# Optimization experiments

Measured on AMD Instinct MI355X. Metric: run time of the kernel, lower is better.

Reference implementation:

```python
import jax, jax.numpy as jnp
import numpy as np

F_DIM, H, O = 128, 256, 256
NQ, EQ = 64, 512
ND, ED = 50000, 600000

PARAM_SHAPES = [
    ("qW1", (F_DIM, H)), ("qb1", (H,)), ("qW2", (H, H)), ("qb2", (H,)),
    ("qW3", (H, H)),     ("qb3", (H,)), ("qW4", (H, O)), ("qb4", (O,)),
    ("dW1", (F_DIM, H)), ("db1", (H,)), ("dW2", (H, H)), ("db2", (H,)),
    ("dW3", (H, H)),     ("db3", (H,)), ("dW4", (H, O)), ("db4", (O,)),
    ("lW1", (2 * O, O)), ("lb1", (O,)),
    ("lW2", (O, O // 2)), ("lb2", (O // 2,)),
    ("lW3", (O // 2, 8)), ("lb3", (8,)),
]

def setup_inputs() -> dict:
    key = jax.random.key(0)
    ks = jax.random.split(key, 4 + len(PARAM_SHAPES))
    inp = {
        "query_in_feat": jax.random.normal(ks[0], (NQ, F_DIM), jnp.float32),
        "data_in_feat": jax.random.normal(ks[1], (ND, F_DIM), jnp.float32),
        "query_edge_list": jax.random.randint(ks[2], (2, EQ), 0, NQ),
        "data_edge_list": jax.random.randint(ks[3], (2, ED), 0, ND),
    }
    for i, (name, shape) in enumerate(PARAM_SHAPES):
        fan_in = shape[0] if len(shape) == 2 else 1
        inp[name] = jax.random.normal(ks[4 + i], shape, jnp.float32) * (1.0 / np.sqrt(fan_in))
    return inp

def _mlp2(x, W1, b1, W2, b2):
    return jnp.maximum(x @ W1 + b1, 0.0) @ W2 + b2

def _gin_conv(x, src, dst, W1, b1, W2, b2):
    # GINConv (eps=0): MLP(x_i + sum_{j->i} x_j); gather x[src], scatter-add at dst
    agg = jax.ops.segment_sum(x[src], dst, num_segments=x.shape[0])
    return _mlp2(x + agg, W1, b1, W2, b2)

def _gin(x, edge_index, p):
    src, dst = edge_index[0], edge_index[1]
    h = jnp.maximum(_gin_conv(x, src, dst, *p[:4]), 0.0)  # ReLU between convs
    return _gin_conv(h, src, dst, *p[4:])

def reference(query_in_feat, data_in_feat, query_edge_list, data_edge_list,
              qW1, qb1, qW2, qb2, qW3, qb3, qW4, qb4,
              dW1, db1, dW2, db2, dW3, db3, dW4, db4,
              lW1, lb1, lW2, lb2, lW3, lb3):
    qx = _gin(query_in_feat, query_edge_list, (qW1, qb1, qW2, qb2, qW3, qb3, qW4, qb4))
    dx = _gin(data_in_feat, data_edge_list, (dW1, db1, dW2, db2, dW3, db3, dW4, db4))
    # global_add_pool with batch = zeros -> single-graph sum
    qp = jnp.sum(qx, axis=0, keepdims=True)  # [1, O]
    dp = jnp.sum(dx, axis=0, keepdims=True)  # [1, O]
    h = jnp.concatenate([qp, dp], axis=1)    # [1, 2*O]
    h = jnp.maximum(h @ lW1 + lb1, 0.0)
    h = jnp.maximum(h @ lW2 + lb2, 0.0)
    h = jnp.maximum(h @ lW3 + lb3, 0.0)
    return h.reshape(1, 8)
```

## Files before the change

kernel.cpp:

```cpp
#include <hip/hip_runtime.h>
#include <hip/hip_bf16.h>


#define NQ 64
#define EQ 512
#define ND 50000
#define ED 600000
#define FDIM 128
#define HDIM 256

typedef __attribute__((ext_vector_type(8))) short short8;
typedef __attribute__((ext_vector_type(4))) float f32x4;
typedef __attribute__((ext_vector_type(4))) unsigned short us4;
typedef __attribute__((ext_vector_type(2))) unsigned short us2;

__device__ __forceinline__ unsigned short f2bf(float f) {
    union { float f; unsigned u; } v; v.f = f;
    unsigned r = v.u + 0x7FFF + ((v.u >> 16) & 1);
    return (unsigned short)(r >> 16);
}
__device__ __forceinline__ float bf2f(unsigned short u) {
    union { unsigned u; float f; } v; v.u = ((unsigned)u) << 16;
    return v.f;
}


__global__ void cvt_to_bf16(const float* __restrict__ xd, const float* __restrict__ xq,
                            unsigned short* __restrict__ out, long long nd4, long long n4) {
    long long i = (long long)blockIdx.x * 256 + threadIdx.x;
    if (i >= n4) return;
    const float* src = (i < nd4) ? (xd + i * 4) : (xq + (i - nd4) * 4);
    float4 v = *(const float4*)src;
    us4 o;
    o[0] = f2bf(v.x); o[1] = f2bf(v.y); o[2] = f2bf(v.z); o[3] = f2bf(v.w);
    *(us4*)(out + i * 4) = o;
}


__global__ void count_deg_both(const int* __restrict__ d_dst, int* __restrict__ d_deg,
                               const int* __restrict__ q_dst, int* __restrict__ q_deg,
                               int dblocks) {
    int b = blockIdx.x;
    if (b < dblocks) {
        int e = b * 256 + threadIdx.x;
        if (e < ED) atomicAdd(&d_deg[d_dst[e]], 1);
    } else {
        int e = (b - dblocks) * 256 + threadIdx.x;
        if (e < EQ) atomicAdd(&q_deg[q_dst[e]], 1);
    }
}

__device__ __forceinline__ void scan1_body(const int* deg, int* rowptr, int* bsum,
                                           int n, int blk) {
    __shared__ int sh[256];
    const int t = threadIdx.x;
    const int i = blk * 256 + t;
    const int v = (i < n) ? deg[i] : 0;
    sh[t] = v;
    __syncthreads();
    for (int off = 1; off < 256; off <<= 1) {
        int x = (t >= off) ? sh[t - off] : 0;
        __syncthreads();
        sh[t] += x;
        __syncthreads();
    }
    if (i < n) rowptr[i] = sh[t] - v;
    if (t == 255) bsum[blk] = sh[255];
}

__global__ void scan_phase1_both(const int* __restrict__ d_deg, int* __restrict__ d_rowptr,
                                 int* __restrict__ d_bsum,
                                 const int* __restrict__ q_deg, int* __restrict__ q_rowptr,
                                 int* __restrict__ q_bsum, int dblocks) {
    int b = blockIdx.x;
    if (b < dblocks) scan1_body(d_deg, d_rowptr, d_bsum, ND, b);
    else             scan1_body(q_deg, q_rowptr, q_bsum, NQ, b - dblocks);
}

__device__ __forceinline__ void scan2_body(const int* bsum, int* boff, int* rowptr_n, int nb) {
    __shared__ int sh[256];
    const int t = threadIdx.x;
    const int v = (t < nb) ? bsum[t] : 0;
    sh[t] = v;
    __syncthreads();
    for (int off = 1; off < 256; off <<= 1) {
        int x = (t >= off) ? sh[t - off] : 0;
        __syncthreads();
        sh[t] += x;
        __syncthreads();
    }
    if (t < nb) boff[t] = sh[t] - v;
    if (t == 255) *rowptr_n = sh[255];
}

__global__ void scan_phase2_both(const int* __restrict__ d_bsum, int* __restrict__ d_boff,
                                 int* __restrict__ d_rowptr_n, int d_nb,
                                 const int* __restrict__ q_bsum, int* __restrict__ q_boff,
                                 int* __restrict__ q_rowptr_n, int q_nb) {
    if (blockIdx.x == 0) scan2_body(d_bsum, d_boff, d_rowptr_n, d_nb);
    else                 scan2_body(q_bsum, q_boff, q_rowptr_n, q_nb);
}

__global__ void scan_phase3_both(int* __restrict__ d_rowptr, const int* __restrict__ d_boff,
                                 int* __restrict__ d_cursor,
                                 int* __restrict__ q_rowptr, const int* __restrict__ q_boff,
                                 int* __restrict__ q_cursor, int dblocks) {
    int b = blockIdx.x;
    if (b < dblocks) {
        int i = b * 256 + threadIdx.x;
        if (i < ND) {
            int r = d_rowptr[i] + d_boff[b];
            d_rowptr[i] = r; d_cursor[i] = r;
        }
    } else {
        int i = (b - dblocks) * 256 + threadIdx.x;
        if (i < NQ) {
            int r = q_rowptr[i] + q_boff[b - dblocks];
            q_rowptr[i] = r; q_cursor[i] = r;
        }
    }
}

__global__ void fill_csr_both(const int* __restrict__ d_src, const int* __restrict__ d_dst,
                              int* __restrict__ d_cursor, int* __restrict__ d_csrsrc,
                              const int* __restrict__ q_src, const int* __restrict__ q_dst,
                              int* __restrict__ q_cursor, int* __restrict__ q_csrsrc,
                              int dblocks) {
    int b = blockIdx.x;
    if (b < dblocks) {
        int e = b * 256 + threadIdx.x;
        if (e < ED) {
            int p = atomicAdd(&d_cursor[d_dst[e]], 1);
            d_csrsrc[p] = d_src[e];
        }
    } else {
        int e = (b - dblocks) * 256 + threadIdx.x;
        if (e < EQ) {
            int p = atomicAdd(&q_cursor[q_dst[e]], 1);
            q_csrsrc[p] = q_src[e];
        }
    }
}


template <int F>
__global__ void gin_agg_dual(const unsigned short* __restrict__ xd, const int* __restrict__ rpd,
                             const int* __restrict__ csd, unsigned short* __restrict__ od,
                             const unsigned short* __restrict__ xq, const int* __restrict__ rpq,
                             const int* __restrict__ csq, unsigned short* __restrict__ oq) {
    constexpr int V = F / 64;
    const unsigned short* x; const int* rowptr; const int* csr; unsigned short* out; int node;
    if ((int)blockIdx.x < ND) { x = xd; rowptr = rpd; csr = csd; out = od; node = blockIdx.x; }
    else { x = xq; rowptr = rpq; csr = csq; out = oq; node = blockIdx.x - ND; }

    const int t = threadIdx.x;
    const int beg = rowptr[node];
    const int end = rowptr[node + 1];

    float acc[V];
    {
        const unsigned short* p = x + (size_t)node * F + t * V;
        if constexpr (V == 4) {
            us4 v = *(const us4*)p;
#pragma unroll
            for (int i = 0; i < 4; ++i) acc[i] = bf2f(v[i]);
        } else {
            us2 v = *(const us2*)p;
            acc[0] = bf2f(v[0]); acc[1] = bf2f(v[1]);
        }
    }
    int j = beg;
    for (; j + 1 < end; j += 2) {
        const unsigned short* p0 = x + (size_t)csr[j] * F + t * V;
        const unsigned short* p1 = x + (size_t)csr[j + 1] * F + t * V;
        if constexpr (V == 4) {
            us4 v0 = *(const us4*)p0;
            us4 v1 = *(const us4*)p1;
#pragma unroll
            for (int i = 0; i < 4; ++i) acc[i] += bf2f(v0[i]) + bf2f(v1[i]);
        } else {
            us2 v0 = *(const us2*)p0;
            us2 v1 = *(const us2*)p1;
            acc[0] += bf2f(v0[0]) + bf2f(v1[0]);
            acc[1] += bf2f(v0[1]) + bf2f(v1[1]);
        }
    }
    if (j < end) {
        const unsigned short* p0 = x + (size_t)csr[j] * F + t * V;
        if constexpr (V == 4) {
            us4 v0 = *(const us4*)p0;
#pragma unroll
            for (int i = 0; i < 4; ++i) acc[i] += bf2f(v0[i]);
        } else {
            us2 v0 = *(const us2*)p0;
            acc[0] += bf2f(v0[0]); acc[1] += bf2f(v0[1]);
        }
    }
    unsigned short* po = out + (size_t)node * F + t * V;
    if constexpr (V == 4) {
        us4 r;
#pragma unroll
        for (int i = 0; i < 4; ++i) r[i] = f2bf(acc[i]);
        *(us4*)po = r;
    } else {
        us2 r; r[0] = f2bf(acc[0]); r[1] = f2bf(acc[1]);
        *(us2*)po = r;
    }
}


struct PackDesc {
    const float* W[8];
    unsigned short* Wp[8];
    int KT[8];
    int start[9];
};

__global__ void pack_all(PackDesc pd) {
    int b = blockIdx.x;
    int m = 0;
    while (m < 7 && b >= pd.start[m + 1]) ++m;
    const int local = b - pd.start[m];
    const int KT = pd.KT[m];
    const int kt = local % KT;
    const int ct = local / KT;
    const float* W = pd.W[m];
    unsigned short* Wp = pd.Wp[m];
    const int l = threadIdx.x;
    const int row = kt * 32 + (l >> 4) * 8;
    const int col = ct * 16 + (l & 15);
    short8 v;
#pragma unroll
    for (int j = 0; j < 8; ++j) v[j] = (short)f2bf(W[(size_t)(row + j) * 256 + col]);
    *(short8*)(Wp + (((size_t)(ct * KT + kt)) * 64 + l) * 8) = v;
}


template <int KIN>
__global__ __launch_bounds__(256) void mlp_dual(
    const unsigned short* __restrict__ Ad,
    const unsigned short* __restrict__ W1pd, const float* __restrict__ b1d,
    const unsigned short* __restrict__ W2pd, const float* __restrict__ b2d,
    unsigned short* __restrict__ Cd, float* __restrict__ poold, int ndb,
    const unsigned short* __restrict__ Aq,
    const unsigned short* __restrict__ W1pq, const float* __restrict__ b1q,
    const unsigned short* __restrict__ W2pq, const float* __restrict__ b2q,
    unsigned short* __restrict__ Cq, float* __restrict__ poolq,
    int relu_out) {
    constexpr int KT1 = KIN / 32;
    __shared__ __align__(16) unsigned short lds[64 * 256];

    const unsigned short* A; const unsigned short* W1p; const float* b1;
    const unsigned short* W2p; const float* b2;
    unsigned short* C; float* pool; int row0, N;
    if ((int)blockIdx.x < ndb) {
        A = Ad; W1p = W1pd; b1 = b1d; W2p = W2pd; b2 = b2d;
        C = Cd; pool = poold; row0 = blockIdx.x * 64; N = ND;
    } else {
        A = Aq; W1p = W1pq; b1 = b1q; W2p = W2pq; b2 = b2q;
        C = Cq; pool = poolq; row0 = 0; N = NQ;
    }

    const int tid = threadIdx.x;
    const int lane = tid & 63;
    const int wv = tid >> 6;
    const int lrow = lane & 15;
    const int lk2 = (lane >> 4) * 8;
    const int nrows = (N - row0 < 64) ? (N - row0) : 64;

    for (int idx = tid; idx < nrows * (KIN / 8); idx += 256) {
        const int r = idx / (KIN / 8);
        const int k8 = (idx % (KIN / 8)) * 8;
        short8 v = *(const short8*)(A + (size_t)(row0 + r) * KIN + k8);
        unsigned byte = (unsigned)((r * KIN + k8) * 2) ^ (unsigned)((r & 7) << 4);
        *(short8*)((char*)lds + byte) = v;
    }
    __syncthreads();

    f32x4 acc1[4][4];
#pragma unroll
    for (int fm = 0; fm < 4; ++fm)
#pragma unroll
        for (int fn = 0; fn < 4; ++fn) acc1[fm][fn] = (f32x4)(0.f);

    const unsigned short* W1Base = W1p + ((size_t)(wv * 4) * KT1 * 64 + lane) * 8;
    for (int kt = 0; kt < KT1; ++kt) {
        short8 a[4], bf[4];
#pragma unroll
        for (int fm = 0; fm < 4; ++fm) {
            const int r = fm * 16 + lrow;
            unsigned byte = (unsigned)((r * KIN + kt * 32 + lk2) * 2) ^ (unsigned)((r & 7) << 4);
            a[fm] = *(const short8*)((const char*)lds + byte);
        }
#pragma unroll
        for (int fn = 0; fn < 4; ++fn)
            bf[fn] = *(const short8*)(W1Base + ((size_t)fn * KT1 + kt) * 64 * 8);
#pragma unroll
        for (int fm = 0; fm < 4; ++fm)
#pragma unroll
            for (int fn = 0; fn < 4; ++fn)
                acc1[fm][fn] = __builtin_amdgcn_mfma_f32_16x16x32_bf16(
                    a[fm], bf[fn], acc1[fm][fn], 0, 0, 0);
    }
    __syncthreads();

#pragma unroll
    for (int fn = 0; fn < 4; ++fn) {
        const int col = wv * 64 + fn * 16 + lrow;
        const float bv = b1[col];
#pragma unroll
        for (int fm = 0; fm < 4; ++fm) {
            const int rbase = fm * 16 + (lane >> 4) * 4;
#pragma unroll
            for (int r = 0; r < 4; ++r) {
                const int row = rbase + r;
                const float v = fmaxf(acc1[fm][fn][r] + bv, 0.f);
                unsigned byte = (unsigned)((row * 256 + col) * 2) ^ (unsigned)((row & 7) << 4);
                *(unsigned short*)((char*)lds + byte) = f2bf(v);
            }
        }
    }
    __syncthreads();

    f32x4 acc2[4][4];
#pragma unroll
    for (int fm = 0; fm < 4; ++fm)
#pragma unroll
        for (int fn = 0; fn < 4; ++fn) acc2[fm][fn] = (f32x4)(0.f);

    const unsigned short* W2Base = W2p + ((size_t)(wv * 4) * 8 * 64 + lane) * 8;
    for (int kt = 0; kt < 8; ++kt) {
        short8 a[4], bf[4];
#pragma unroll
        for (int fm = 0; fm < 4; ++fm) {
            const int r = fm * 16 + lrow;
            unsigned byte = (unsigned)((r * 256 + kt * 32 + lk2) * 2) ^ (unsigned)((r & 7) << 4);
            a[fm] = *(const short8*)((const char*)lds + byte);
        }
#pragma unroll
        for (int fn = 0; fn < 4; ++fn)
            bf[fn] = *(const short8*)(W2Base + ((size_t)fn * 8 + kt) * 64 * 8);
#pragma unroll
        for (int fm = 0; fm < 4; ++fm)
#pragma unroll
            for (int fn = 0; fn < 4; ++fn)
                acc2[fm][fn] = __builtin_amdgcn_mfma_f32_16x16x32_bf16(
                    a[fm], bf[fn], acc2[fm][fn], 0, 0, 0);
    }

#pragma unroll
    for (int fn = 0; fn < 4; ++fn) {
        const int col = wv * 64 + fn * 16 + lrow;
        const float bv = b2[col];
        float ps = 0.f;
#pragma unroll
        for (int fm = 0; fm < 4; ++fm) {
            const int rbase = row0 + fm * 16 + (lane >> 4) * 4;
#pragma unroll
            for (int r = 0; r < 4; ++r) {
                const int row = rbase + r;
                if (row < N) {
                    float v = acc2[fm][fn][r] + bv;
                    if (relu_out) v = fmaxf(v, 0.f);
                    if (C) C[(size_t)row * 256 + col] = f2bf(v);
                    ps += v;
                }
            }
        }
        if (pool) {
            ps += __shfl_xor(ps, 16);
            ps += __shfl_xor(ps, 32);
            if ((lane >> 4) == 0) atomicAdd(&pool[col], ps);
        }
    }
}


__global__ void mlp_head(const float* __restrict__ pooled,
                         const float* __restrict__ lW1, const float* __restrict__ lb1,
                         const float* __restrict__ lW2, const float* __restrict__ lb2,
                         const float* __restrict__ lW3, const float* __restrict__ lb3,
                         float* __restrict__ out) {
    __shared__ float h0[512];
    __shared__ float h1[256];
    __shared__ float h2[128];
    const int t = threadIdx.x;
    h0[t] = pooled[t];
    h0[t + 256] = pooled[t + 256];
    __syncthreads();

    float acc = lb1[t];
    for (int k = 0; k < 512; ++k) acc += h0[k] * lW1[k * 256 + t];
    h1[t] = fmaxf(acc, 0.f);
    __syncthreads();

    if (t < 128) {
        float a = lb2[t];
        for (int k = 0; k < 256; ++k) a += h1[k] * lW2[k * 128 + t];
        h2[t] = fmaxf(a, 0.f);
    }
    __syncthreads();

    if (t < 8) {
        float a = lb3[t];
        for (int k = 0; k < 128; ++k) a += h2[k] * lW3[k * 8 + t];
        out[t] = fmaxf(a, 0.f);
    }
}


extern "C" void kernel_launch(void* const* d_in, const int* in_sizes, int n_in,
                              void* d_out, int out_size, void* d_ws, size_t ws_size,
                              hipStream_t stream) {
    const float* q_x  = (const float*)d_in[0];
    const float* d_x  = (const float*)d_in[1];
    const int*   q_el = (const int*)d_in[2];
    const int*   d_el = (const int*)d_in[3];
    const float* qW1 = (const float*)d_in[4];  const float* qb1 = (const float*)d_in[5];
    const float* qW2 = (const float*)d_in[6];  const float* qb2 = (const float*)d_in[7];
    const float* qW3 = (const float*)d_in[8];  const float* qb3 = (const float*)d_in[9];
    const float* qW4 = (const float*)d_in[10]; const float* qb4 = (const float*)d_in[11];
    const float* dW1 = (const float*)d_in[12]; const float* db1 = (const float*)d_in[13];
    const float* dW2 = (const float*)d_in[14]; const float* db2 = (const float*)d_in[15];
    const float* dW3 = (const float*)d_in[16]; const float* db3 = (const float*)d_in[17];
    const float* dW4 = (const float*)d_in[18]; const float* db4 = (const float*)d_in[19];
    const float* lW1 = (const float*)d_in[20]; const float* lb1 = (const float*)d_in[21];
    const float* lW2 = (const float*)d_in[22]; const float* lb2 = (const float*)d_in[23];
    const float* lW3 = (const float*)d_in[24]; const float* lb3 = (const float*)d_in[25];
    (void)in_sizes; (void)n_in; (void)out_size; (void)ws_size;

    const int* q_src = q_el;  const int* q_dst = q_el + EQ;
    const int* d_src = d_el;  const int* d_dst = d_el + ED;

    char* wsb = (char*)d_ws;
    size_t off = 0;
    auto alloc = [&](size_t bytes) { void* p = wsb + off; off += (bytes + 255) & ~(size_t)255; return p; };

    unsigned short* bxd = (unsigned short*)alloc((size_t)ND * FDIM * 2);
    unsigned short* bxq = (unsigned short*)alloc((size_t)NQ * FDIM * 2);
    unsigned short* dag = (unsigned short*)alloc((size_t)ND * FDIM * 2);
    unsigned short* qag = (unsigned short*)alloc((size_t)NQ * FDIM * 2);
    unsigned short* hd  = (unsigned short*)alloc((size_t)ND * HDIM * 2);
    unsigned short* hq  = (unsigned short*)alloc((size_t)NQ * HDIM * 2);
    unsigned short* had = (unsigned short*)alloc((size_t)ND * HDIM * 2);
    unsigned short* haq = (unsigned short*)alloc((size_t)NQ * HDIM * 2);
    float* pooled = (float*)alloc(512 * 4);
    int* d_deg    = (int*)alloc((size_t)ND * 4);
    int* q_deg    = (int*)alloc((size_t)NQ * 4);
    int* d_rowptr = (int*)alloc((size_t)(ND + 1) * 4);
    int* d_cursor = (int*)alloc((size_t)ND * 4);
    int* d_csrsrc = (int*)alloc((size_t)ED * 4);
    int* d_bsum   = (int*)alloc(256 * 4);
    int* d_boff   = (int*)alloc(256 * 4);
    int* q_rowptr = (int*)alloc((size_t)(NQ + 1) * 4);
    int* q_cursor = (int*)alloc((size_t)NQ * 4);
    int* q_csrsrc = (int*)alloc((size_t)EQ * 4);
    int* q_bsum   = (int*)alloc(256 * 4);
    int* q_boff   = (int*)alloc(256 * 4);
    unsigned short* pdW1 = (unsigned short*)alloc((size_t)FDIM * 256 * 2);
    unsigned short* pdW2 = (unsigned short*)alloc((size_t)HDIM * 256 * 2);
    unsigned short* pdW3 = (unsigned short*)alloc((size_t)HDIM * 256 * 2);
    unsigned short* pdW4 = (unsigned short*)alloc((size_t)HDIM * 256 * 2);
    unsigned short* pqW1 = (unsigned short*)alloc((size_t)FDIM * 256 * 2);
    unsigned short* pqW2 = (unsigned short*)alloc((size_t)HDIM * 256 * 2);
    unsigned short* pqW3 = (unsigned short*)alloc((size_t)HDIM * 256 * 2);
    unsigned short* pqW4 = (unsigned short*)alloc((size_t)HDIM * 256 * 2);

    hipMemsetAsync(pooled, 0, 512 * 4, stream);
    hipMemsetAsync(d_deg, 0, (char*)(q_deg + NQ) - (char*)d_deg, stream);

    {
        long long nd4 = (long long)ND * FDIM / 4;
        long long n4 = nd4 + (long long)NQ * FDIM / 4;
        cvt_to_bf16<<<(int)((n4 + 255) / 256), 256, 0, stream>>>(d_x, q_x, bxd, nd4, n4);
    }

    {
        PackDesc pd;
        const float* Ws[8] = {dW1, dW2, dW3, dW4, qW1, qW2, qW3, qW4};
        unsigned short* Wps[8] = {pdW1, pdW2, pdW3, pdW4, pqW1, pqW2, pqW3, pqW4};
        int kts[8] = {4, 8, 8, 8, 4, 8, 8, 8};
        int s = 0;
        for (int i = 0; i < 8; ++i) {
            pd.W[i] = Ws[i]; pd.Wp[i] = Wps[i]; pd.KT[i] = kts[i];
            pd.start[i] = s; s += 16 * kts[i];
        }
        pd.start[8] = s;
        pack_all<<<s, 64, 0, stream>>>(pd);
    }

    const int d_eb = (ED + 255) / 256;
    const int q_eb = (EQ + 255) / 256;
    const int d_nb = (ND + 255) / 256;
    const int q_nb = (NQ + 255) / 256;
    count_deg_both<<<d_eb + q_eb, 256, 0, stream>>>(d_dst, d_deg, q_dst, q_deg, d_eb);
    scan_phase1_both<<<d_nb + q_nb, 256, 0, stream>>>(d_deg, d_rowptr, d_bsum,
                                                      q_deg, q_rowptr, q_bsum, d_nb);
    scan_phase2_both<<<2, 256, 0, stream>>>(d_bsum, d_boff, d_rowptr + ND, d_nb,
                                            q_bsum, q_boff, q_rowptr + NQ, q_nb);
    scan_phase3_both<<<d_nb + q_nb, 256, 0, stream>>>(d_rowptr, d_boff, d_cursor,
                                                      q_rowptr, q_boff, q_cursor, d_nb);
    fill_csr_both<<<d_eb + q_eb, 256, 0, stream>>>(d_src, d_dst, d_cursor, d_csrsrc,
                                                   q_src, q_dst, q_cursor, q_csrsrc, d_eb);

    const int ndb = (ND + 63) / 64;

    gin_agg_dual<FDIM><<<ND + NQ, 64, 0, stream>>>(bxd, d_rowptr, d_csrsrc, dag,
                                                   bxq, q_rowptr, q_csrsrc, qag);
    mlp_dual<FDIM><<<ndb + 1, 256, 0, stream>>>(
        dag, pdW1, db1, pdW2, db2, hd, nullptr, ndb,
        qag, pqW1, qb1, pqW2, qb2, hq, nullptr, 1);

    gin_agg_dual<HDIM><<<ND + NQ, 64, 0, stream>>>(hd, d_rowptr, d_csrsrc, had,
                                                   hq, q_rowptr, q_csrsrc, haq);
    mlp_dual<HDIM><<<ndb + 1, 256, 0, stream>>>(
        had, pdW3, db3, pdW4, db4, nullptr, pooled + 256, ndb,
        haq, pqW3, qb3, pqW4, qb4, nullptr, pooled, 0);

    mlp_head<<<1, 256, 0, stream>>>(pooled, lW1, lb1, lW2, lb2, lW3, lb3, (float*)d_out);
}
```

Before: 260.9 us.

## Store hidden activations as FP8 and fuse prepass kernels into one launch

The intermediate hidden features between the two GIN layers are now stored as FP8 (one byte per element) instead of bf16. A new aggregation kernel gathers and sums them with packed fp8-to-f32 conversion, which halves the bytes moved in the memory-bound neighbor gather and in the MLP output write. Separately, feature conversion, weight packing and degree counting are merged into a single prepass launch to cut launch overhead. FP8 storage of activations loses precision and may push accuracy toward the tolerance limit, and the MLP now writes single bytes per lane, which is less coalesced.

```diff
diff --git a/kernel.cpp b/kernel.cpp
--- a/kernel.cpp
+++ b/kernel.cpp
@@ -11,6 +11,7 @@
 
 typedef __attribute__((ext_vector_type(8))) short short8;
 typedef __attribute__((ext_vector_type(4))) float f32x4;
+typedef __attribute__((ext_vector_type(2))) float floatx2;
 typedef __attribute__((ext_vector_type(4))) unsigned short us4;
 typedef __attribute__((ext_vector_type(2))) unsigned short us2;
 
@@ -25,30 +26,62 @@
 }
 
 
-__global__ void cvt_to_bf16(const float* __restrict__ xd, const float* __restrict__ xq,
-                            unsigned short* __restrict__ out, long long nd4, long long n4) {
-    long long i = (long long)blockIdx.x * 256 + threadIdx.x;
-    if (i >= n4) return;
-    const float* src = (i < nd4) ? (xd + i * 4) : (xq + (i - nd4) * 4);
-    float4 v = *(const float4*)src;
-    us4 o;
-    o[0] = f2bf(v.x); o[1] = f2bf(v.y); o[2] = f2bf(v.z); o[3] = f2bf(v.w);
-    *(us4*)(out + i * 4) = o;
-}
-
-
-__global__ void count_deg_both(const int* __restrict__ d_dst, int* __restrict__ d_deg,
-                               const int* __restrict__ q_dst, int* __restrict__ q_deg,
-                               int dblocks) {
-    int b = blockIdx.x;
-    if (b < dblocks) {
-        int e = b * 256 + threadIdx.x;
-        if (e < ED) atomicAdd(&d_deg[d_dst[e]], 1);
+struct PackDesc {
+    const float* W[8];
+    unsigned short* Wp[8];
+    int KT[8];
+    int start[9];
+};
+
+__device__ __forceinline__ void pack_unit(const PackDesc& pd, int unit, int l) {
+    int m = 0;
+    while (m < 7 && unit >= pd.start[m + 1]) ++m;
+    const int local = unit - pd.start[m];
+    const int KT = pd.KT[m];
+    const int kt = local % KT;
+    const int ct = local / KT;
+    const float* W = pd.W[m];
+    unsigned short* Wp = pd.Wp[m];
+    const int row = kt * 32 + (l >> 4) * 8;
+    const int col = ct * 16 + (l & 15);
+    short8 v;
+#pragma unroll
+    for (int j = 0; j < 8; ++j) v[j] = (short)f2bf(W[(size_t)(row + j) * 256 + col]);
+    *(short8*)(Wp + (((size_t)(ct * KT + kt)) * 64 + l) * 8) = v;
+}
+
+
+__global__ void prepass(const float* __restrict__ xd, const float* __restrict__ xq,
+                        unsigned short* __restrict__ bx, long long nd4, long long n4,
+                        int cvt_b, PackDesc pd, int pack_units, int pack_b,
+                        const int* __restrict__ d_dst, int* __restrict__ d_deg,
+                        const int* __restrict__ q_dst, int* __restrict__ q_deg,
+                        int d_eb) {
+    const int b = blockIdx.x;
+    const int tid = threadIdx.x;
+    if (b < cvt_b) {
+        long long i = (long long)b * 256 + tid;
+        if (i >= n4) return;
+        const float* src = (i < nd4) ? (xd + i * 4) : (xq + (i - nd4) * 4);
+        float4 v = *(const float4*)src;
+        us4 o;
+        o[0] = f2bf(v.x); o[1] = f2bf(v.y); o[2] = f2bf(v.z); o[3] = f2bf(v.w);
+        *(us4*)(bx + i * 4) = o;
+    } else if (b < cvt_b + pack_b) {
+        const int unit = (b - cvt_b) * 4 + (tid >> 6);
+        if (unit < pack_units) pack_unit(pd, unit, tid & 63);
     } else {
-        int e = (b - dblocks) * 256 + threadIdx.x;
-        if (e < EQ) atomicAdd(&q_deg[q_dst[e]], 1);
-    }
-}
+        const int cb = b - cvt_b - pack_b;
+        if (cb < d_eb) {
+            int e = cb * 256 + tid;
+            if (e < ED) atomicAdd(&d_deg[d_dst[e]], 1);
+        } else {
+            int e = (cb - d_eb) * 256 + tid;
+            if (e < EQ) atomicAdd(&q_deg[q_dst[e]], 1);
+        }
+    }
+}
+
 
 __device__ __forceinline__ void scan1_body(const int* deg, int* rowptr, int* bsum,
                                            int n, int blk) {
@@ -209,30 +242,45 @@
 }
 
 
-struct PackDesc {
-    const float* W[8];
-    unsigned short* Wp[8];
-    int KT[8];
-    int start[9];
-};
-
-__global__ void pack_all(PackDesc pd) {
-    int b = blockIdx.x;
-    int m = 0;
-    while (m < 7 && b >= pd.start[m + 1]) ++m;
-    const int local = b - pd.start[m];
-    const int KT = pd.KT[m];
-    const int kt = local % KT;
-    const int ct = local / KT;
-    const float* W = pd.W[m];
-    unsigned short* Wp = pd.Wp[m];
-    const int l = threadIdx.x;
-    const int row = kt * 32 + (l >> 4) * 8;
-    const int col = ct * 16 + (l & 15);
-    short8 v;
-#pragma unroll
-    for (int j = 0; j < 8; ++j) v[j] = (short)f2bf(W[(size_t)(row + j) * 256 + col]);
-    *(short8*)(Wp + (((size_t)(ct * KT + kt)) * 64 + l) * 8) = v;
+__global__ void gin_agg_f8_dual(const unsigned char* __restrict__ xd, const int* __restrict__ rpd,
+                                const int* __restrict__ csd, unsigned short* __restrict__ od,
+                                const unsigned char* __restrict__ xq, const int* __restrict__ rpq,
+                                const int* __restrict__ csq, unsigned short* __restrict__ oq) {
+    const unsigned char* x; const int* rowptr; const int* csr; unsigned short* out; int node;
+    if ((int)blockIdx.x < ND) { x = xd; rowptr = rpd; csr = csd; out = od; node = blockIdx.x; }
+    else { x = xq; rowptr = rpq; csr = csq; out = oq; node = blockIdx.x - ND; }
+
+    const int t = threadIdx.x;
+    const int beg = rowptr[node];
+    const int end = rowptr[node + 1];
+
+    float a0, a1, a2, a3;
+    {
+        const unsigned w = *(const unsigned*)(x + (size_t)node * 256 + t * 4);
+        floatx2 lo = __builtin_amdgcn_cvt_pk_f32_fp8((int)w, false);
+        floatx2 hi = __builtin_amdgcn_cvt_pk_f32_fp8((int)w, true);
+        a0 = lo[0]; a1 = lo[1]; a2 = hi[0]; a3 = hi[1];
+    }
+    int j = beg;
+    for (; j + 1 < end; j += 2) {
+        const unsigned w0 = *(const unsigned*)(x + (size_t)csr[j] * 256 + t * 4);
+        const unsigned w1 = *(const unsigned*)(x + (size_t)csr[j + 1] * 256 + t * 4);
+        floatx2 l0 = __builtin_amdgcn_cvt_pk_f32_fp8((int)w0, false);
+        floatx2 h0 = __builtin_amdgcn_cvt_pk_f32_fp8((int)w0, true);
+        floatx2 l1 = __builtin_amdgcn_cvt_pk_f32_fp8((int)w1, false);
+        floatx2 h1 = __builtin_amdgcn_cvt_pk_f32_fp8((int)w1, true);
+        a0 += l0[0] + l1[0]; a1 += l0[1] + l1[1];
+        a2 += h0[0] + h1[0]; a3 += h0[1] + h1[1];
+    }
+    if (j < end) {
+        const unsigned w0 = *(const unsigned*)(x + (size_t)csr[j] * 256 + t * 4);
+        floatx2 l0 = __builtin_amdgcn_cvt_pk_f32_fp8((int)w0, false);
+        floatx2 h0 = __builtin_amdgcn_cvt_pk_f32_fp8((int)w0, true);
+        a0 += l0[0]; a1 += l0[1]; a2 += h0[0]; a3 += h0[1];
+    }
+    us4 r;
+    r[0] = f2bf(a0); r[1] = f2bf(a1); r[2] = f2bf(a2); r[3] = f2bf(a3);
+    *(us4*)(out + (size_t)node * 256 + t * 4) = r;
 }
 
 
@@ -241,24 +289,24 @@
     const unsigned short* __restrict__ Ad,
     const unsigned short* __restrict__ W1pd, const float* __restrict__ b1d,
     const unsigned short* __restrict__ W2pd, const float* __restrict__ b2d,
-    unsigned short* __restrict__ Cd, float* __restrict__ poold, int ndb,
+    unsigned char* __restrict__ C8d, float* __restrict__ poold, int ndb,
     const unsigned short* __restrict__ Aq,
     const unsigned short* __restrict__ W1pq, const float* __restrict__ b1q,
     const unsigned short* __restrict__ W2pq, const float* __restrict__ b2q,
-    unsigned short* __restrict__ Cq, float* __restrict__ poolq,
+    unsigned char* __restrict__ C8q, float* __restrict__ poolq,
     int relu_out) {
     constexpr int KT1 = KIN / 32;
     __shared__ __align__(16) unsigned short lds[64 * 256];
 
     const unsigned short* A; const unsigned short* W1p; const float* b1;
     const unsigned short* W2p; const float* b2;
-    unsigned short* C; float* pool; int row0, N;
+    unsigned char* C8; float* pool; int row0, N;
     if ((int)blockIdx.x < ndb) {
         A = Ad; W1p = W1pd; b1 = b1d; W2p = W2pd; b2 = b2d;
-        C = Cd; pool = poold; row0 = blockIdx.x * 64; N = ND;
+        C8 = C8d; pool = poold; row0 = blockIdx.x * 64; N = ND;
     } else {
         A = Aq; W1p = W1pq; b1 = b1q; W2p = W2pq; b2 = b2q;
-        C = Cq; pool = poolq; row0 = 0; N = NQ;
+        C8 = C8q; pool = poolq; row0 = 0; N = NQ;
     }
 
     const int tid = threadIdx.x;
@@ -362,7 +410,10 @@
                 if (row < N) {
                     float v = acc2[fm][fn][r] + bv;
                     if (relu_out) v = fmaxf(v, 0.f);
-                    if (C) C[(size_t)row * 256 + col] = f2bf(v);
+                    if (C8) {
+                        unsigned p = (unsigned)__builtin_amdgcn_cvt_pk_fp8_f32(v, v, 0, false);
+                        C8[(size_t)row * 256 + col] = (unsigned char)(p & 0xff);
+                    }
                     ps += v;
                 }
             }
@@ -440,8 +491,8 @@
     unsigned short* bxq = (unsigned short*)alloc((size_t)NQ * FDIM * 2);
     unsigned short* dag = (unsigned short*)alloc((size_t)ND * FDIM * 2);
     unsigned short* qag = (unsigned short*)alloc((size_t)NQ * FDIM * 2);
-    unsigned short* hd  = (unsigned short*)alloc((size_t)ND * HDIM * 2);
-    unsigned short* hq  = (unsigned short*)alloc((size_t)NQ * HDIM * 2);
+    unsigned char*  h8d = (unsigned char*)alloc((size_t)ND * HDIM);
+    unsigned char*  h8q = (unsigned char*)alloc((size_t)NQ * HDIM);
     unsigned short* had = (unsigned short*)alloc((size_t)ND * HDIM * 2);
     unsigned short* haq = (unsigned short*)alloc((size_t)NQ * HDIM * 2);
     float* pooled = (float*)alloc(512 * 4);
@@ -469,12 +520,10 @@
     hipMemsetAsync(pooled, 0, 512 * 4, stream);
     hipMemsetAsync(d_deg, 0, (char*)(q_deg + NQ) - (char*)d_deg, stream);
 
-    {
-        long long nd4 = (long long)ND * FDIM / 4;
-        long long n4 = nd4 + (long long)NQ * FDIM / 4;
-        cvt_to_bf16<<<(int)((n4 + 255) / 256), 256, 0, stream>>>(d_x, q_x, bxd, nd4, n4);
-    }
-
+    const int d_eb = (ED + 255) / 256;
+    const int q_eb = (EQ + 255) / 256;
+    const int d_nb = (ND + 255) / 256;
+    const int q_nb = (NQ + 255) / 256;
     {
         PackDesc pd;
         const float* Ws[8] = {dW1, dW2, dW3, dW4, qW1, qW2, qW3, qW4};
@@ -486,14 +535,16 @@
             pd.start[i] = s; s += 16 * kts[i];
         }
         pd.start[8] = s;
-        pack_all<<<s, 64, 0, stream>>>(pd);
-    }
-
-    const int d_eb = (ED + 255) / 256;
-    const int q_eb = (EQ + 255) / 256;
-    const int d_nb = (ND + 255) / 256;
-    const int q_nb = (NQ + 255) / 256;
-    count_deg_both<<<d_eb + q_eb, 256, 0, stream>>>(d_dst, d_deg, q_dst, q_deg, d_eb);
+        const int pack_units = s;
+        const int pack_b = (s + 3) / 4;
+        long long nd4 = (long long)ND * FDIM / 4;
+        long long n4 = nd4 + (long long)NQ * FDIM / 4;
+        const int cvt_b = (int)((n4 + 255) / 256);
+        prepass<<<cvt_b + pack_b + d_eb + q_eb, 256, 0, stream>>>(
+            d_x, q_x, bxd, nd4, n4, cvt_b, pd, pack_units, pack_b,
+            d_dst, d_deg, q_dst, q_deg, d_eb);
+    }
+
     scan_phase1_both<<<d_nb + q_nb, 256, 0, stream>>>(d_deg, d_rowptr, d_bsum,
                                                       q_deg, q_rowptr, q_bsum, d_nb);
     scan_phase2_both<<<2, 256, 0, stream>>>(d_bsum, d_boff, d_rowptr + ND, d_nb,
@@ -508,11 +559,11 @@
     gin_agg_dual<FDIM><<<ND + NQ, 64, 0, stream>>>(bxd, d_rowptr, d_csrsrc, dag,
                                                    bxq, q_rowptr, q_csrsrc, qag);
     mlp_dual<FDIM><<<ndb + 1, 256, 0, stream>>>(
-        dag, pdW1, db1, pdW2, db2, hd, nullptr, ndb,
-        qag, pqW1, qb1, pqW2, qb2, hq, nullptr, 1);
-
-    gin_agg_dual<HDIM><<<ND + NQ, 64, 0, stream>>>(hd, d_rowptr, d_csrsrc, had,
-                                                   hq, q_rowptr, q_csrsrc, haq);
+        dag, pdW1, db1, pdW2, db2, h8d, nullptr, ndb,
+        qag, pqW1, qb1, pqW2, qb2, h8q, nullptr, 1);
+
+    gin_agg_f8_dual<<<ND + NQ, 64, 0, stream>>>(h8d, d_rowptr, d_csrsrc, had,
+                                                h8q, q_rowptr, q_csrsrc, haq);
     mlp_dual<HDIM><<<ndb + 1, 256, 0, stream>>>(
         had, pdW3, db3, pdW4, db4, nullptr, pooled + 256, ndb,
         haq, pqW3, qb3, pqW4, qb4, nullptr, pooled, 0);
```

Measured after the change: 236.4 us. 1.1x faster.
